# Kernel optimization log

Hardware: AMD Instinct MI355X
Metric: run time of the kernel (lower is better)

The kernel has to match this reference:

```python
import jax, jax.numpy as jnp
import numpy as np

PC = (-60.0, -60.0, -4.0, 140.0, 60.0, 4.0)
BEV_H, BEV_W, E, HEADS, LVLS, PTS, ZN, CAMS = 50, 50, 256, 8, 3, 4, 4, 6
HD = E // HEADS
IMG_H, IMG_W = 512.0, 800.0
SHAPES = ((64, 100), (32, 50), (16, 25))
FFN = 2 * E
EPS = 1e-5


def grid_sample(img, grid):
    # img (B,C,H,W), grid (B,Hg,Wg,2) in [-1,1]; bilinear, zeros padding, align_corners=False
    B, C, H, W = img.shape
    Hg, Wg = grid.shape[1], grid.shape[2]
    x = (grid[..., 0] + 1.0) * (W * 0.5) - 0.5
    y = (grid[..., 1] + 1.0) * (H * 0.5) - 0.5
    x0 = jnp.floor(x)
    y0 = jnp.floor(y)
    wx = x - x0
    wy = y - y0
    x0i = x0.astype(jnp.int32)
    y0i = y0.astype(jnp.int32)
    imgf = img.reshape(B, C, H * W)

    def gather(ix, iy):
        valid = ((ix >= 0) & (ix < W) & (iy >= 0) & (iy < H)).astype(img.dtype)
        idx = jnp.clip(iy, 0, H - 1) * W + jnp.clip(ix, 0, W - 1)
        idx = jnp.broadcast_to(idx.reshape(B, 1, Hg * Wg), (B, C, Hg * Wg))
        return jnp.take_along_axis(imgf, idx, axis=2).reshape(B, C, Hg, Wg) * valid[:, None]

    v00 = gather(x0i, y0i)
    v01 = gather(x0i + 1, y0i)
    v10 = gather(x0i, y0i + 1)
    v11 = gather(x0i + 1, y0i + 1)
    wx = wx[:, None]
    wy = wy[:, None]
    return v00 * (1 - wy) * (1 - wx) + v01 * (1 - wy) * wx + v10 * wy * (1 - wx) + v11 * wy * wx


def layer_norm(x, g, b):
    m = x.mean(-1, keepdims=True)
    v = ((x - m) ** 2).mean(-1, keepdims=True)
    return (x - m) / jnp.sqrt(v + 1e-5) * g + b


def get_reference_points():
    xs = (jnp.arange(BEV_W, dtype=jnp.float32) + 0.5) / BEV_W
    ys = (jnp.arange(BEV_H, dtype=jnp.float32) + 0.5) / BEV_H
    zs = (jnp.arange(ZN, dtype=jnp.float32) + 0.5) / ZN
    ref_y, ref_x = jnp.meshgrid(ys, xs, indexing='ij')
    xy = jnp.stack([ref_x, ref_y], -1).reshape(-1, 2)  # (HW,2)
    xy = jnp.broadcast_to(xy[:, None, :], (BEV_H * BEV_W, ZN, 2))
    z = jnp.broadcast_to(zs[None, :, None], (BEV_H * BEV_W, ZN, 1))
    r = jnp.concatenate([xy, z], -1)  # (HW,Z,3), normalized
    scale = jnp.array([PC[3] - PC[0], PC[4] - PC[1], PC[5] - PC[2]], jnp.float32)
    off = jnp.array([PC[0], PC[1], PC[2]], jnp.float32)
    return (r * scale + off).reshape(-1, 3)  # (HW*Z, 3)


def point_sampling(ref3d, l2i):
    # ref3d (Nq,3), l2i (B,N,4,4) -> ref2d (B,N,Nq,2), mask (B,N,Nq)
    Nq = ref3d.shape[0]
    pts = jnp.concatenate([ref3d, jnp.ones((Nq, 1), ref3d.dtype)], -1)
    cam = jnp.einsum('bnij,qj->bnqi', l2i, pts)
    d = cam[..., 2]
    u = cam[..., 0] / (d + EPS) / IMG_W
    v = cam[..., 1] / (d + EPS) / IMG_H
    ref2d = jnp.stack([u, v], -1)
    mask = (d > EPS) & (u > 0.0) & (u < 1.0) & (v > 0.0) & (v < 1.0)
    return ref2d, mask


def mha(q, k, v, fl):
    B = q.shape[0]
    wq, wk, wv = jnp.split(fl['ta_in_w'], 3, 0)
    bq, bk, bv = jnp.split(fl['ta_in_b'], 3, 0)
    Q = (q @ wq.T + bq).reshape(B, -1, HEADS, HD)
    K = (k @ wk.T + bk).reshape(B, -1, HEADS, HD)
    V = (v @ wv.T + bv).reshape(B, -1, HEADS, HD)
    a = jax.nn.softmax(jnp.einsum('bqhd,bkhd->bhqk', Q, K) / np.float32(np.sqrt(HD)), -1)
    o = jnp.einsum('bhqk,bkhd->bqhd', a, V).reshape(B, -1, E)
    return o @ fl['ta_out_w'].T + fl['ta_out_b']


def msda(query, qpos, value, ref, fl):
    # MultiScaleDeformableAttention (identity = zeros). ref (B,Nq,L,2) in [0,1].
    B, Nq, _ = query.shape
    q = query + qpos
    v = (value @ fl['vp_w'].T + fl['vp_b']).reshape(B, -1, HEADS, HD)
    off = (q @ fl['so_w'].T + fl['so_b']).reshape(B, Nq, HEADS, LVLS, PTS, 2)
    aw = jax.nn.softmax((q @ fl['aw_w'].T + fl['aw_b']).reshape(B, Nq, HEADS, LVLS * PTS), -1)
    aw = aw.reshape(B, Nq, HEADS, LVLS, PTS)
    norm = jnp.array([[w, h] for (h, w) in SHAPES], jnp.float32)  # (L,2) = (W,H)
    loc = ref[:, :, None, :, None, :] + off / norm[None, None, None, :, None, :]
    outs = []
    start = 0
    for l, (Hl, Wl) in enumerate(SHAPES):
        vl = v[:, start:start + Hl * Wl].transpose(0, 2, 3, 1).reshape(B * HEADS, HD, Hl, Wl)
        g = (2.0 * loc[:, :, :, l] - 1.0).transpose(0, 2, 1, 3, 4).reshape(B * HEADS, Nq, PTS, 2)
        outs.append(grid_sample(vl, g))  # (B*HEADS, HD, Nq, PTS)
        start += Hl * Wl
    s = jnp.stack(outs, 3)  # (B*HEADS, HD, Nq, L, P)
    w = aw.transpose(0, 2, 1, 3, 4).reshape(B * HEADS, 1, Nq, LVLS, PTS)
    o = (s * w).sum((3, 4)).reshape(B, HEADS, HD, Nq).transpose(0, 3, 1, 2).reshape(B, Nq, E)
    return o @ fl['op_w'].T + fl['op_b']


def spatial_attn(query, qpos, feats_t, l2i, ref3d, fl):
    B, Nq, _ = query.shape
    ref2d, mask = point_sampling(ref3d, l2i)
    out = jnp.zeros_like(query)
    valid = jnp.zeros((B, Nq), query.dtype)
    for cam in range(CAMS):
        value = jnp.concatenate(
            [f[:, cam].reshape(B, E, -1).transpose(0, 2, 1) for f in feats_t], axis=1)
        ref = jnp.broadcast_to(ref2d[:, cam][:, :, None, :], (B, Nq, LVLS, 2))
        a = msda(query, qpos, value, ref, fl)
        wgt = mask[:, cam].astype(query.dtype)
        out = out + a * wgt[..., None]
        valid = valid + wgt
    return out / jnp.maximum(valid, 1.0)[..., None]


def temporal_align(prev_bev, motion):
    B, C, H, W = prev_bev.shape
    xs = jnp.arange(W, dtype=prev_bev.dtype)
    ys = jnp.arange(H, dtype=prev_bev.dtype)
    yy, xx = jnp.meshgrid(ys, xs, indexing='ij')
    rx = (xx + 0.5) / W * (PC[3] - PC[0]) + PC[0]
    ry = (yy + 0.5) / H * (PC[4] - PC[1]) + PC[1]
    g = jnp.stack([rx, ry, jnp.zeros_like(rx), jnp.ones_like(rx)], -1)  # (H,W,4)
    inv = jnp.linalg.inv(motion)  # (B,4,4)
    gp = jnp.einsum('bij,hwj->bhwi', inv, g)
    nx = (gp[..., 0] - PC[0]) / (PC[3] - PC[0]) * 2.0 - 1.0
    ny = (gp[..., 1] - PC[1]) / (PC[4] - PC[1]) * 2.0 - 1.0
    return grid_sample(prev_bev, jnp.stack([nx, ny], -1))


def layer_fwd(bev, bev_pos, prev, feats_t, l2i, ref3d, fl):
    if prev is not None:
        attn = mha(bev + bev_pos, prev + bev_pos, prev, fl)
        bev = layer_norm(bev + attn, fl['n1_g'], fl['n1_b'])
    B, Nq, C = bev.shape
    bev_z = jnp.broadcast_to(bev[:, :, None, :], (B, Nq, ZN, C)).reshape(B, -1, C)
    pos_z = jnp.broadcast_to(bev_pos[:, :, None, :], (B, Nq, ZN, C)).reshape(B, -1, C)
    so = spatial_attn(bev_z, pos_z, feats_t, l2i, ref3d, fl)
    so = so.reshape(B, Nq, ZN, C).mean(2)
    bev = layer_norm(bev + so, fl['n2_g'], fl['n2_b'])
    h = jax.nn.relu(bev @ fl['ffn_w1'].T + fl['ffn_b1'])
    ffn = h @ fl['ffn_w2'].T + fl['ffn_b2']
    return layer_norm(bev + ffn, fl['n3_g'], fl['n3_b'])


def forward(fl, batch_size, seq_len):
    feats = [fl['feat0'], fl['feat1'], fl['feat2']]
    feats = [f.reshape(batch_size, seq_len, CAMS, E, f.shape[-2], f.shape[-1]) for f in feats]
    bev = jnp.broadcast_to(fl['bev_emb'][None], (batch_size, BEV_H * BEV_W, E))
    bev_pos = jnp.broadcast_to(fl['bev_pos_emb'][None], (batch_size, BEV_H * BEV_W, E))
    ref3d = get_reference_points()
    prev = None
    for t in range(seq_len):
        feats_t = [f[:, t] for f in feats]
        prev_al = None
        if prev is not None:
            pa = temporal_align(prev, fl['ego_motion'][:, t])
            prev_al = pa.reshape(batch_size, E, -1).transpose(0, 2, 1)
        bev_t = layer_fwd(bev, bev_pos, prev_al, feats_t, fl['lidar2img'][:, t], ref3d, fl)
        prev = bev_t.transpose(0, 2, 1).reshape(batch_size, E, BEV_H, BEV_W)
    return prev


def _make_cam_matrices():
    mats = np.zeros((CAMS, 4, 4), np.float32)
    K = np.array([[500.0, 0.0, 400.0], [0.0, 500.0, 256.0], [0.0, 0.0, 1.0]], np.float32)
    for i in range(CAMS):
        th = 2.0 * np.pi * i / CAMS
        xr = np.array([-np.sin(th), np.cos(th), 0.0])
        yr = np.array([0.0, 0.0, -1.0])
        fr = np.array([np.cos(th), np.sin(th), 0.0])
        R = np.stack([xr, yr, fr]).astype(np.float32)
        mats[i, :3, :3] = K @ R
        mats[i, 3, 3] = 1.0
    return mats


def setup_inputs() -> dict:
    key = jax.random.key(0)
    ks = jax.random.split(key, 20)
    rn = lambda k, s, sc=0.02: jax.random.normal(k, s, jnp.float32) * sc
    NOFF = HEADS * LVLS * PTS * 2
    NAW = HEADS * LVLS * PTS
    d = {
        'bev_emb': rn(ks[0], (BEV_H * BEV_W, E), 1.0),
        'bev_pos_emb': rn(ks[1], (BEV_H * BEV_W, E), 1.0),
        'ta_in_w': rn(ks[2], (3 * E, E)), 'ta_in_b': jnp.zeros(3 * E, jnp.float32),
        'ta_out_w': rn(ks[3], (E, E)), 'ta_out_b': jnp.zeros(E, jnp.float32),
        'so_w': rn(ks[4], (NOFF, E)), 'so_b': rn(ks[5], (NOFF,), 0.5),
        'aw_w': rn(ks[6], (NAW, E)), 'aw_b': jnp.zeros(NAW, jnp.float32),
        'vp_w': rn(ks[7], (E, E)), 'vp_b': jnp.zeros(E, jnp.float32),
        'op_w': rn(ks[8], (E, E)), 'op_b': jnp.zeros(E, jnp.float32),
        'ffn_w1': rn(ks[9], (FFN, E)), 'ffn_b1': jnp.zeros(FFN, jnp.float32),
        'ffn_w2': rn(ks[10], (E, FFN)), 'ffn_b2': jnp.zeros(E, jnp.float32),
        'n1_g': jnp.ones(E, jnp.float32), 'n1_b': jnp.zeros(E, jnp.float32),
        'n2_g': jnp.ones(E, jnp.float32), 'n2_b': jnp.zeros(E, jnp.float32),
        'n3_g': jnp.ones(E, jnp.float32), 'n3_b': jnp.zeros(E, jnp.float32),
        'feat0': rn(ks[11], (12, E, 64, 100), 1.0),
        'feat1': rn(ks[12], (12, E, 32, 50), 1.0),
        'feat2': rn(ks[13], (12, E, 16, 25), 1.0),
    }
    mats = _make_cam_matrices()  # realistic lidar->img projections per camera
    d['lidar2img'] = jnp.asarray(np.broadcast_to(mats, (1, 2, CAMS, 4, 4)).copy())
    em = np.tile(np.eye(4, dtype=np.float32), (1, 2, 1, 1))
    em[..., 0, 3] = 2.0  # 2m forward ego translation per step
    d['ego_motion'] = jnp.asarray(em)
    d['batch_size'] = 1
    d['seq_len'] = 2
    return d


def reference(bev_emb, bev_pos_emb, ta_in_w, ta_in_b, ta_out_w, ta_out_b,
              so_w, so_b, aw_w, aw_b, vp_w, vp_b, op_w, op_b,
              ffn_w1, ffn_b1, ffn_w2, ffn_b2,
              n1_g, n1_b, n2_g, n2_b, n3_g, n3_b,
              feat0, feat1, feat2, lidar2img, ego_motion, batch_size, seq_len):
    fl = dict(bev_emb=bev_emb, bev_pos_emb=bev_pos_emb, ta_in_w=ta_in_w, ta_in_b=ta_in_b,
              ta_out_w=ta_out_w, ta_out_b=ta_out_b, so_w=so_w, so_b=so_b, aw_w=aw_w, aw_b=aw_b,
              vp_w=vp_w, vp_b=vp_b, op_w=op_w, op_b=op_b, ffn_w1=ffn_w1, ffn_b1=ffn_b1,
              ffn_w2=ffn_w2, ffn_b2=ffn_b2, n1_g=n1_g, n1_b=n1_b, n2_g=n2_g, n2_b=n2_b,
              n3_g=n3_g, n3_b=n3_b, feat0=feat0, feat1=feat1, feat2=feat2,
              lidar2img=lidar2img, ego_motion=ego_motion)
    return forward(fl, int(batch_size), int(seq_len))
```

## Files before the change

### kernel.cpp

```cpp
#include <hip/hip_runtime.h>
#include <hip/hip_bf16.h>

#define NPIX   2500
#define EDIM   256
#define NHEADS 8
#define HDIM   32
#define NLVLS  3
#define NPTS   4
#define NZ     4
#define NCAMS  6
#define NQTOT  10000
#define NVAL   8400
#define FFND   512
#define NCHUNK 10
#define KVCH   250
#define VTROW  2504

typedef __attribute__((ext_vector_type(8))) short short8;
typedef __attribute__((ext_vector_type(4))) float float4v;

__device__ __forceinline__ void level_params(int l, int& H, int& W, int& st) {
    if (l == 0)      { H = 64; W = 100; st = 0;    }
    else if (l == 1) { H = 32; W = 50;  st = 6400; }
    else             { H = 16; W = 25;  st = 8000; }
// ... 88 lines not shown
        {
            const int gw = n0 + srow;
            if (gw < N) {
                const float* src = Wf + (size_t)gw * K + k0 + sk;
#pragma unroll
                for (int j = 0; j < 8; j++) tmp[j] = f2bf(src[j]);
            } else {
#pragma unroll
                for (int j = 0; j < 8; j++) tmp[j] = 0;
            }
            *(short8*)&Ws[srow][sk] = *(short8*)&tmp[0];
        }
        __syncthreads();
        short8 af[2], bfr[2];
#pragma unroll
        for (int mi = 0; mi < 2; mi++)
            af[mi] = *(const short8*)&As[wr * 32 + mi * 16 + fr][fk * 8];
#pragma unroll
        for (int ni = 0; ni < 2; ni++)
            bfr[ni] = *(const short8*)&Ws[wc * 32 + ni * 16 + fr][fk * 8];
#pragma unroll
        for (int mi = 0; mi < 2; mi++)
#pragma unroll
            for (int ni = 0; ni < 2; ni++)
                acc[mi][ni] = __builtin_amdgcn_mfma_f32_16x16x32_bf16(
                    af[mi], bfr[ni], acc[mi][ni], 0, 0, 0);
        __syncthreads();
    }
#pragma unroll
    for (int mi = 0; mi < 2; mi++)
#pragma unroll
        for (int ni = 0; ni < 2; ni++) {
            const int col = n0 + wc * 32 + ni * 16 + fr;
#pragma unroll
            for (int r = 0; r < 4; r++) {
                const int row = m0 + wr * 32 + mi * 16 + fk * 4 + r;
                if (row < M && col < N) {
                    float v = acc[mi][ni][r] + (Bf ? Bf[col] : 0.f);
                    if (ACT) v = fmaxf(v, 0.f);
                    Cb[(size_t)row * N + col] = v;
                }
            }
        }
}

template<int ACT, int ADD>
__global__ __launch_bounds__(256) void gemm64o_k(const float* __restrict__ A,
                                                 const float* __restrict__ A2,
                                                 const float* __restrict__ W,
                                                 const float* __restrict__ bias,
                                                 unsigned short* __restrict__ C,
                                                 int M, int N, int K)
{
    __shared__ unsigned short As[64][44];
    __shared__ unsigned short Ws[64][44];
    const int m0 = blockIdx.y * 64;
    const int n0 = blockIdx.x * 64;
    const int tid = threadIdx.x;
    const int wave = tid >> 6, lane = tid & 63;
    const int wr = wave >> 1, wc = wave & 1;
    const int fr = lane & 15, fk = lane >> 4;
    float4v acc[2][2];
#pragma unroll
    for (int mi = 0; mi < 2; mi++)
#pragma unroll
        for (int ni = 0; ni < 2; ni++) { acc[mi][ni][0] = 0.f; acc[mi][ni][1] = 0.f;
                                         acc[mi][ni][2] = 0.f; acc[mi][ni][3] = 0.f; }
    const int srow = tid >> 2, sk = (tid & 3) * 8;
    for (int k0 = 0; k0 < K; k0 += 32) {
        unsigned short tmp[8];
        {
            const int gr = m0 + srow;
            if (gr < M) {
                const float* src = A + (size_t)gr * K + k0 + sk;
                if (ADD) {
                    const float* src2 = A2 + (size_t)gr * K + k0 + sk;
#pragma unroll
                    for (int j = 0; j < 8; j++) tmp[j] = f2bf(src[j] + src2[j]);
                } else {
#pragma unroll
                    for (int j = 0; j < 8; j++) tmp[j] = f2bf(src[j]);
                }
            } else {
#pragma unroll
                for (int j = 0; j < 8; j++) tmp[j] = 0;
            }
            *(short8*)&As[srow][sk] = *(short8*)&tmp[0];
        }
        {
            const int gw = n0 + srow;
            if (gw < N) {
                const float* src = W + (size_t)gw * K + k0 + sk;
#pragma unroll
                for (int j = 0; j < 8; j++) tmp[j] = f2bf(src[j]);
            } else {
#pragma unroll
                for (int j = 0; j < 8; j++) tmp[j] = 0;
            }
            *(short8*)&Ws[srow][sk] = *(short8*)&tmp[0];
        }
        __syncthreads();
        short8 af[2], bfr[2];
#pragma unroll
        for (int mi = 0; mi < 2; mi++)
            af[mi] = *(const short8*)&As[wr * 32 + mi * 16 + fr][fk * 8];
#pragma unroll
        for (int ni = 0; ni < 2; ni++)
            bfr[ni] = *(const short8*)&Ws[wc * 32 + ni * 16 + fr][fk * 8];
#pragma unroll
        for (int mi = 0; mi < 2; mi++)
#pragma unroll
            for (int ni = 0; ni < 2; ni++)
                acc[mi][ni] = __builtin_amdgcn_mfma_f32_16x16x32_bf16(
                    af[mi], bfr[ni], acc[mi][ni], 0, 0, 0);
        __syncthreads();
    }
#pragma unroll
    for (int mi = 0; mi < 2; mi++)
#pragma unroll
        for (int ni = 0; ni < 2; ni++) {
            const int col = n0 + wc * 32 + ni * 16 + fr;
#pragma unroll
            for (int r = 0; r < 4; r++) {
                const int row = m0 + wr * 32 + mi * 16 + fk * 4 + r;
                if (row < M && col < N) {
                    float v = acc[mi][ni][r] + (bias ? bias[col] : 0.f);
                    if (ACT) v = fmaxf(v, 0.f);
                    C[(size_t)row * N + col] = f2bf(v);
                }
            }
        }
}

__global__ __launch_bounds__(256) void gemm_qkv_k(const float* __restrict__ bev_emb,
                                                  const float* __restrict__ prev_al,
                                                  const float* __restrict__ bev_pose,
                                                  const float* __restrict__ ta_in_w,
                                                  const float* __restrict__ ta_in_b,
                                                  unsigned short* __restrict__ Qbf,
                                                  unsigned short* __restrict__ Kbf,
                                                  unsigned short* __restrict__ VbfT)
{
    __shared__ unsigned short As[64][44];
    __shared__ unsigned short Ws[64][44];
    const int z = blockIdx.z;
    const float* A    = (z == 0) ? bev_emb : prev_al;
    const float* A2   = (z == 2) ? nullptr : bev_pose;
    const float* W    = ta_in_w + (size_t)z * EDIM * EDIM;
    const float* bias = ta_in_b + z * EDIM;
    const float oscale = (z == 0) ? 0.17677669529663689f : 1.0f;
    unsigned short* C = (z == 0) ? Qbf : (z == 1) ? Kbf : VbfT;
    const int m0 = blockIdx.y * 64;
    const int n0 = blockIdx.x * 64;
    const int tid = threadIdx.x;
    const int wave = tid >> 6, lane = tid & 63;
    const int wr = wave >> 1, wc = wave & 1;
    const int fr = lane & 15, fk = lane >> 4;
    float4v acc[2][2];
#pragma unroll
    for (int mi = 0; mi < 2; mi++)
#pragma unroll
        for (int ni = 0; ni < 2; ni++) { acc[mi][ni][0] = 0.f; acc[mi][ni][1] = 0.f;
                                         acc[mi][ni][2] = 0.f; acc[mi][ni][3] = 0.f; }
    const int srow = tid >> 2, sk = (tid & 3) * 8;
    for (int k0 = 0; k0 < EDIM; k0 += 32) {
        unsigned short tmp[8];
        {
            const int gr = m0 + srow;
            if (gr < NPIX) {
                const float* src = A + (size_t)gr * EDIM + k0 + sk;
                if (A2) {
                    const float* src2 = A2 + (size_t)gr * EDIM + k0 + sk;
#pragma unroll
                    for (int j = 0; j < 8; j++) tmp[j] = f2bf(src[j] + src2[j]);
                } else {
#pragma unroll
                    for (int j = 0; j < 8; j++) tmp[j] = f2bf(src[j]);
                }
            } else {
#pragma unroll
                for (int j = 0; j < 8; j++) tmp[j] = 0;
            }
            *(short8*)&As[srow][sk] = *(short8*)&tmp[0];
        }
        {
            const float* src = W + (size_t)(n0 + srow) * EDIM + k0 + sk;
#pragma unroll
            for (int j = 0; j < 8; j++) tmp[j] = f2bf(src[j]);
            *(short8*)&Ws[srow][sk] = *(short8*)&tmp[0];
        }
        __syncthreads();
        short8 af[2], bfr[2];
#pragma unroll
        for (int mi = 0; mi < 2; mi++)
            af[mi] = *(const short8*)&As[wr * 32 + mi * 16 + fr][fk * 8];
#pragma unroll
        for (int ni = 0; ni < 2; ni++)
            bfr[ni] = *(const short8*)&Ws[wc * 32 + ni * 16 + fr][fk * 8];
#pragma unroll
        for (int mi = 0; mi < 2; mi++)
#pragma unroll
            for (int ni = 0; ni < 2; ni++)
                acc[mi][ni] = __builtin_amdgcn_mfma_f32_16x16x32_bf16(
                    af[mi], bfr[ni], acc[mi][ni], 0, 0, 0);
        __syncthreads();
    }
#pragma unroll
    for (int mi = 0; mi < 2; mi++)
#pragma unroll
        for (int ni = 0; ni < 2; ni++) {
            const int col = n0 + wc * 32 + ni * 16 + fr;
#pragma unroll
            for (int r = 0; r < 4; r++) {
                const int row = m0 + wr * 32 + mi * 16 + fk * 4 + r;
                if (row < NPIX) {
                    const float v = (acc[mi][ni][r] + bias[col]) * oscale;
                    if (z == 2)
                        C[(size_t)col * VTROW + row] = f2bf(v);
                    else
                        C[(size_t)row * EDIM + col] = f2bf(v);
                }
            }
        }
}

__global__ __launch_bounds__(256) void gemm64b_k(const unsigned short* __restrict__ A,
                                                 const float* __restrict__ W,
                                                 const float* __restrict__ bias,
                                                 float* __restrict__ C,
                                                 int M, int N, int K,
                                                 size_t a_bs, size_t c_bs)
{
    __shared__ unsigned short As[64][44];
    __shared__ unsigned short Ws[64][44];
    const int m0 = blockIdx.y * 64;
    const int n0 = blockIdx.x * 64;
    const int tid = threadIdx.x;
    const unsigned short* Af = A + blockIdx.z * a_bs;
    float* Cb = C + blockIdx.z * c_bs;
    const int wave = tid >> 6, lane = tid & 63;
    const int wr = wave >> 1, wc = wave & 1;
    const int fr = lane & 15, fk = lane >> 4;
    float4v acc[2][2];
#pragma unroll
    for (int mi = 0; mi < 2; mi++)
#pragma unroll
        for (int ni = 0; ni < 2; ni++) { acc[mi][ni][0] = 0.f; acc[mi][ni][1] = 0.f;
                                         acc[mi][ni][2] = 0.f; acc[mi][ni][3] = 0.f; }
    const int srow = tid >> 2, sk = (tid & 3) * 8;
    for (int k0 = 0; k0 < K; k0 += 32) {
        {
            const int gr = m0 + srow;
            if (gr < M) {
                *(short8*)&As[srow][sk] =
                    *(const short8*)&Af[(size_t)gr * K + k0 + sk];
            } else {
                short8 z = {0,0,0,0,0,0,0,0};
                *(short8*)&As[srow][sk] = z;
            }
        }
        {
            unsigned short tmp[8];
            const int gw = n0 + srow;
            if (gw < N) {
                const float* src = W + (size_t)gw * K + k0 + sk;
#pragma unroll
                for (int j = 0; j < 8; j++) tmp[j] = f2bf(src[j]);
            } else {
#pragma unroll
                for (int j = 0; j < 8; j++) tmp[j] = 0;
            }
            *(short8*)&Ws[srow][sk] = *(short8*)&tmp[0];
        }
        __syncthreads();
        short8 af[2], bfr[2];
#pragma unroll
        for (int mi = 0; mi < 2; mi++)
            af[mi] = *(const short8*)&As[wr * 32 + mi * 16 + fr][fk * 8];
#pragma unroll
        for (int ni = 0; ni < 2; ni++)
            bfr[ni] = *(const short8*)&Ws[wc * 32 + ni * 16 + fr][fk * 8];
#pragma unroll
        for (int mi = 0; mi < 2; mi++)
#pragma unroll
            for (int ni = 0; ni < 2; ni++)
                acc[mi][ni] = __builtin_amdgcn_mfma_f32_16x16x32_bf16(
                    af[mi], bfr[ni], acc[mi][ni], 0, 0, 0);
        __syncthreads();
    }
#pragma unroll
    for (int mi = 0; mi < 2; mi++)
#pragma unroll
        for (int ni = 0; ni < 2; ni++) {
            const int col = n0 + wc * 32 + ni * 16 + fr;
#pragma unroll
            for (int r = 0; r < 4; r++) {
                const int row = m0 + wr * 32 + mi * 16 + fk * 4 + r;
                if (row < M && col < N)
                    Cb[(size_t)row * N + col] = acc[mi][ni][r] + (bias ? bias[col] : 0.f);
            }
        }
}

__global__ __launch_bounds__(256) void gemm_soaw_k(const float* __restrict__ A,
                                                   const float* __restrict__ A2,
                                                   const float* __restrict__ Wso,
                                                   const float* __restrict__ Waw,
                                                   const float* __restrict__ Bso,
                                                   const float* __restrict__ Baw,
                                                   float* __restrict__ C)
{
    __shared__ unsigned short As[64][44];
    __shared__ unsigned short Ws[64][44];
    const int m0 = blockIdx.y * 64;
    const int n0 = blockIdx.x * 64;
    const int tid = threadIdx.x;
    const int wave = tid >> 6, lane = tid & 63;
    const int wr = wave >> 1, wc = wave & 1;
    const int fr = lane & 15, fk = lane >> 4;
    float4v acc[2][2];
#pragma unroll
    for (int mi = 0; mi < 2; mi++)
#pragma unroll
        for (int ni = 0; ni < 2; ni++) { acc[mi][ni][0] = 0.f; acc[mi][ni][1] = 0.f;
                                         acc[mi][ni][2] = 0.f; acc[mi][ni][3] = 0.f; }
    const int srow = tid >> 2, sk = (tid & 3) * 8;
    for (int k0 = 0; k0 < EDIM; k0 += 32) {
        unsigned short tmp[8];
        {
            const int gr = m0 + srow;
            if (gr < NPIX) {
                const float* src  = A  + (size_t)gr * EDIM + k0 + sk;
                const float* src2 = A2 + (size_t)gr * EDIM + k0 + sk;
#pragma unroll
                for (int j = 0; j < 8; j++) tmp[j] = f2bf(src[j] + src2[j]);
            } else {
#pragma unroll
                for (int j = 0; j < 8; j++) tmp[j] = 0;
            }
            *(short8*)&As[srow][sk] = *(short8*)&tmp[0];
        }
        {
            const int gw = n0 + srow;
            const float* src = (gw < 192) ? Wso + (size_t)gw * EDIM + k0 + sk
                             : (gw < 288) ? Waw + (size_t)(gw - 192) * EDIM + k0 + sk
                                          : nullptr;
            if (src) {
#pragma unroll
                for (int j = 0; j < 8; j++) tmp[j] = f2bf(src[j]);
            } else {
#pragma unroll
                for (int j = 0; j < 8; j++) tmp[j] = 0;
            }
            *(short8*)&Ws[srow][sk] = *(short8*)&tmp[0];
        }
        __syncthreads();
        short8 af[2], bfr[2];
#pragma unroll
        for (int mi = 0; mi < 2; mi++)
            af[mi] = *(const short8*)&As[wr * 32 + mi * 16 + fr][fk * 8];
#pragma unroll
        for (int ni = 0; ni < 2; ni++)
            bfr[ni] = *(const short8*)&Ws[wc * 32 + ni * 16 + fr][fk * 8];
#pragma unroll
        for (int mi = 0; mi < 2; mi++)
#pragma unroll
            for (int ni = 0; ni < 2; ni++)
                acc[mi][ni] = __builtin_amdgcn_mfma_f32_16x16x32_bf16(
                    af[mi], bfr[ni], acc[mi][ni], 0, 0, 0);
        __syncthreads();
    }
#pragma unroll
    for (int mi = 0; mi < 2; mi++)
#pragma unroll
        for (int ni = 0; ni < 2; ni++) {
            const int col = n0 + wc * 32 + ni * 16 + fr;
#pragma unroll
            for (int r = 0; r < 4; r++) {
                const int row = m0 + wr * 32 + mi * 16 + fk * 4 + r;
                if (row < NPIX && col < 288) {
                    const float b = (col < 192) ? Bso[col] : Baw[col - 192];
                    C[(size_t)row * 288 + col] = acc[mi][ni][r] + b;
                }
            }
        }
}

template<int TRANS>
__global__ __launch_bounds__(256) void resid_ln_k(const float* __restrict__ x0,
                                                  const float* __restrict__ x1,
                                                  const float* __restrict__ cvec,
                                                  const float* __restrict__ cscale,
                                                  const float* __restrict__ g,
                                                  const float* __restrict__ bta,
                                                  float* __restrict__ out)
{
    const int row = blockIdx.x, e = threadIdx.x;
    float x = x0[(size_t)row * EDIM + e] + x1[(size_t)row * EDIM + e];
    if (cvec) x += cvec[e] * cscale[row];
    __shared__ float red[256];
    red[e] = x; __syncthreads();
    for (int s = 128; s > 0; s >>= 1) { if (e < s) red[e] += red[e + s]; __syncthreads(); }
    float mean = red[0] * (1.f / 256.f);
    __syncthreads();
    float dx = x - mean;
    red[e] = dx * dx; __syncthreads();
    for (int s = 128; s > 0; s >>= 1) { if (e < s) red[e] += red[e + s]; __syncthreads(); }
    float var = red[0] * (1.f / 256.f);
    const float res = dx * rsqrtf(var + 1e-5f) * g[e] + bta[e];
    if (TRANS)
        out[(size_t)e * NPIX + row] = res;
    else
        out[(size_t)row * EDIM + e] = res;
}

__global__ void uv_aw_k(const float* __restrict__ l2i, int t,
                        const float* __restrict__ raw,
                        float* __restrict__ uvtab,
                        float* __restrict__ validn,
                        float* __restrict__ aw_soft)
{
    if (blockIdx.x < 40) {
        const int n = blockIdx.x * 256 + threadIdx.x;
        if (n >= NQTOT) return;
        const int pix = n >> 2, iz = n & 3;
        const int prow = pix / 50, pcol = pix % 50;
        const float x3 = (pcol + 0.5f) * 4.0f - 60.f;
        const float y3 = (prow + 0.5f) * 2.4f - 60.f;
        const float z3 = (iz + 0.5f) * 2.0f - 4.f;
        int vcount = 0;
        float buf[12];
#pragma unroll
        for (int cam = 0; cam < NCAMS; cam++) {
            const float* Mt = l2i + (size_t)(t * NCAMS + cam) * 16;
            const float p0 = Mt[0] * x3 + Mt[1] * y3 + Mt[2]  * z3 + Mt[3];
            const float p1 = Mt[4] * x3 + Mt[5] * y3 + Mt[6]  * z3 + Mt[7];
            const float p2 = Mt[8] * x3 + Mt[9] * y3 + Mt[10] * z3 + Mt[11];
            const float dd = p2 + 1e-5f;
            const float u = p0 / dd * (1.f / 800.f);
            const float v = p1 / dd * (1.f / 512.f);
            const bool valid = (p2 > 1e-5f) && (u > 0.f) && (u < 1.f) &&
                               (v > 0.f) && (v < 1.f);
            if (valid) vcount++;
            buf[cam * 2]     = valid ? u : -1.f;
            buf[cam * 2 + 1] = v;
        }
#pragma unroll
        for (int j = 0; j < 12; j++) uvtab[(size_t)n * 12 + j] = buf[j];
        validn[n] = (float)vcount;
    } else {
        const int gidx = (blockIdx.x - 40) * 256 + threadIdx.x;
        if (gidx >= NPIX * NHEADS) return;
        const int pix = gidx / NHEADS, h = gidx % NHEADS;
        const float* p = raw + (size_t)pix * 288 + 192 + h * 12;
        float m = -3.0e38f;
#pragma unroll
        for (int j = 0; j < 12; j++) m = fmaxf(m, p[j]);
        float e[12]; float s = 0.f;
#pragma unroll
        for (int j = 0; j < 12; j++) { e[j] = __expf(p[j] - m); s += e[j]; }
        const float inv = 1.f / s;
        float* o = aw_soft + (size_t)pix * 96 + h * 12;
#pragma unroll
        for (int j = 0; j < 12; j++) o[j] = e[j] * inv;
    }
}

__global__ __launch_bounds__(256) void spatial_sample_k(const float* __restrict__ vproj,
                                                        const float* __restrict__ offb,
                                                        const float* __restrict__ awb,
                                                        const float* __restrict__ uvtab,
                                                        float* __restrict__ S)
{
    const int n = blockIdx.x;
    const int tid = threadIdx.x;
    const int wave = tid >> 6, lane = tid & 63;
    const int ch0 = lane << 2;
    const int h = lane >> 3;
    const int pix = n >> 2;
    __shared__ float soff[192];
    __shared__ float saw[96];
    __shared__ float suv[12];
    __shared__ float red[3][256];
    if (tid < 192) soff[tid] = offb[(size_t)pix * 288 + tid];
    if (tid < 96)  saw[tid]  = awb[(size_t)pix * 96 + tid];
    if (tid >= 192 && tid < 204) suv[tid - 192] = uvtab[(size_t)n * 12 + (tid - 192)];
    __syncthreads();
    float4 acc = make_float4(0.f, 0.f, 0.f, 0.f);
    for (int cam = 0; cam < NCAMS; cam++) {
        const float u = suv[cam * 2];
        if (u < 0.f) continue;
        const float v = suv[cam * 2 + 1];
        const float* vc = vproj + (size_t)cam * NVAL * EDIM + ch0;
        for (int pt = wave; pt < NLVLS * NPTS; pt += 4) {
            const int l = pt >> 2, p = pt & 3;
            int Hl, Wl, st; level_params(l, Hl, Wl, st);
            const int ob = ((h * NLVLS + l) * NPTS + p) * 2;
            const float x = u * (float)Wl + soff[ob]     - 0.5f;
            const float y = v * (float)Hl + soff[ob + 1] - 0.5f;
            const float xf = floorf(x), yf = floorf(y);
            const float wx = x - xf, wy = y - yf;
            const int x0 = (int)xf, y0 = (int)yf;
            const float a = saw[(h * NLVLS + l) * NPTS + p];
            const bool xi0 = (x0 >= 0) & (x0 < Wl);
            const bool xi1 = (x0 + 1 >= 0) & (x0 + 1 < Wl);
            const bool yi0 = (y0 >= 0) & (y0 < Hl);
            const bool yi1 = (y0 + 1 >= 0) & (y0 + 1 < Hl);
            const int rb = st + y0 * Wl + x0;
            float4 sv = make_float4(0.f, 0.f, 0.f, 0.f);
            if (yi0 & xi0) {
                const float w00 = (1.f - wy) * (1.f - wx);
                const float4 t4 = *(const float4*)(vc + ((size_t)rb << 8));
                sv.x += w00 * t4.x; sv.y += w00 * t4.y; sv.z += w00 * t4.z; sv.w += w00 * t4.w;
            }
            if (yi0 & xi1) {
                const float w01 = (1.f - wy) * wx;
                const float4 t4 = *(const float4*)(vc + ((size_t)(rb + 1) << 8));
                sv.x += w01 * t4.x; sv.y += w01 * t4.y; sv.z += w01 * t4.z; sv.w += w01 * t4.w;
            }
            if (yi1 & xi0) {
                const float w10 = wy * (1.f - wx);
                const float4 t4 = *(const float4*)(vc + ((size_t)(rb + Wl) << 8));
                sv.x += w10 * t4.x; sv.y += w10 * t4.y; sv.z += w10 * t4.z; sv.w += w10 * t4.w;
            }
            if (yi1 & xi1) {
                const float w11 = wy * wx;
                const float4 t4 = *(const float4*)(vc + ((size_t)(rb + Wl + 1) << 8));
                sv.x += w11 * t4.x; sv.y += w11 * t4.y; sv.z += w11 * t4.z; sv.w += w11 * t4.w;
            }
            acc.x += a * sv.x; acc.y += a * sv.y; acc.z += a * sv.z; acc.w += a * sv.w;
        }
    }
    if (wave > 0) *(float4*)&red[wave - 1][ch0] = acc;
    __syncthreads();
    if (wave == 0) {
#pragma unroll
        for (int w2 = 0; w2 < 3; w2++) {
            const float4 r4 = *(const float4*)&red[w2][ch0];
            acc.x += r4.x; acc.y += r4.y; acc.z += r4.z; acc.w += r4.w;
        }
        *(float4*)(S + (size_t)n * EDIM + ch0) = acc;
    }
}

__global__ __launch_bounds__(256) void reduce_z_k(const float* __restrict__ S,
                                                  const float* __restrict__ validn,
                                                  unsigned short* __restrict__ Smbf,
                                                  float* __restrict__ vbm)
{
    const int pix = blockIdx.x, e = threadIdx.x;
    float s = 0.f, vb = 0.f;
#pragma unroll
    for (int iz = 0; iz < NZ; iz++) {
        int n = pix * NZ + iz;
        float vn = validn[n];
        float inv = 1.f / fmaxf(vn, 1.f);
        s += S[(size_t)n * EDIM + e] * inv;
        vb += (vn > 0.f) ? 1.f : 0.f;
    }
    Smbf[(size_t)pix * EDIM + e] = f2bf(s * 0.25f);
    if (e == 0) vbm[pix] = vb * 0.25f;
}

__global__ __launch_bounds__(256) void talign_k(const float* __restrict__ prev,
                                                const float* __restrict__ motion,
                                                float* __restrict__ out)
{
    __shared__ float sinv[16];
    if (threadIdx.x == 0) {
        float a[4][8];
        for (int i = 0; i < 4; i++)
            for (int j = 0; j < 4; j++) { a[i][j] = motion[i * 4 + j];
                                          a[i][4 + j] = (i == j) ? 1.f : 0.f; }
        for (int col = 0; col < 4; col++) {
            int piv = col;
            for (int r = col + 1; r < 4; r++)
                if (fabsf(a[r][col]) > fabsf(a[piv][col])) piv = r;
            if (piv != col)
                for (int j = 0; j < 8; j++) { float tp = a[col][j];
                                              a[col][j] = a[piv][j]; a[piv][j] = tp; }
            float idv = 1.f / a[col][col];
            for (int j = 0; j < 8; j++) a[col][j] *= idv;
            for (int r = 0; r < 4; r++) {
                if (r == col) continue;
                float f = a[r][col];
                for (int j = 0; j < 8; j++) a[r][j] -= f * a[col][j];
            }
        }
        for (int i = 0; i < 4; i++)
            for (int j = 0; j < 4; j++) sinv[i * 4 + j] = a[i][4 + j];
    }
    __syncthreads();
    const int pix = blockIdx.x, e = threadIdx.x;
    const int r = pix / 50, c = pix % 50;
    const float rx = (c + 0.5f) * 4.0f - 60.f;
    const float ry = (r + 0.5f) * 2.4f - 60.f;
    const float gx = sinv[0] * rx + sinv[1] * ry + sinv[3];
    const float gy = sinv[4] * rx + sinv[5] * ry + sinv[7];
    const float nx = (gx + 60.f) * 0.01f - 1.f;
    const float ny = (gy + 60.f) * (1.f / 60.f) - 1.f;
    const float x = (nx + 1.f) * 25.f - 0.5f;
    const float y = (ny + 1.f) * 25.f - 0.5f;
    const float xf = floorf(x), yf = floorf(y);
    const float wx = x - xf, wy = y - yf;
    const int x0 = (int)xf, y0 = (int)yf;
    bool xi0 = (x0 >= 0 && x0 < 50), xi1 = (x0 + 1 >= 0 && x0 + 1 < 50);
    bool yi0 = (y0 >= 0 && y0 < 50), yi1 = (y0 + 1 >= 0 && y0 + 1 < 50);
    float s = 0.f;
    if (yi0 && xi0) s += (1.f - wy) * (1.f - wx) * prev[(size_t)(y0 * 50 + x0) * EDIM + e];
    if (yi0 && xi1) s += (1.f - wy) * wx         * prev[(size_t)(y0 * 50 + x0 + 1) * EDIM + e];
    if (yi1 && xi0) s += wy * (1.f - wx)         * prev[(size_t)((y0 + 1) * 50 + x0) * EDIM + e];
    if (yi1 && xi1) s += wy * wx                 * prev[(size_t)((y0 + 1) * 50 + x0 + 1) * EDIM + e];
    out[(size_t)pix * EDIM + e] = s;
}

__global__ __launch_bounds__(256) void mha_mfma_k(const unsigned short* __restrict__ Qbf,
                                                  const unsigned short* __restrict__ Kbf,
                                                  const unsigned short* __restrict__ VbfT,
                                                  float* __restrict__ pacc,
                                                  float* __restrict__ pml)
{
    const int h = blockIdx.y;
    const int q0 = blockIdx.x * 64;
    const int chunk = blockIdx.z;
    const int kv0 = chunk * KVCH;
    const int kv1 = min(NPIX, kv0 + KVCH);
    const int tid = threadIdx.x;
    const int wave = tid >> 6, lane = tid & 63;
    const int fr = lane & 15, fk = lane >> 4;

    __shared__ unsigned short Qs[64][44];
    __shared__ unsigned short Ks[64][44];
    __shared__ unsigned short Vt[32][76];
    __shared__ unsigned short Ps[4][16][76];

    const int srow = tid >> 2, scs = tid & 3;
    {
        const int gq = q0 + srow;
        if (gq < NPIX)
            *(short8*)&Qs[srow][scs * 8] =
                *(const short8*)&Qbf[(size_t)gq * EDIM + h * HDIM + scs * 8];
        else {
            short8 z = {0,0,0,0,0,0,0,0};
            *(short8*)&Qs[srow][scs * 8] = z;
        }
    }
    __syncthreads();
    const short8 aq = *(const short8*)&Qs[wave * 16 + fr][fk * 8];

    float m[4], l[4];
    float4v o0, o1;
#pragma unroll
    for (int r = 0; r < 4; r++) { m[r] = -3.0e38f; l[r] = 0.f; o0[r] = 0.f; o1[r] = 0.f; }

    const int vd = tid >> 3, vpart = tid & 7;
    for (int kb = kv0; kb < kv1; kb += 64) {
        __syncthreads();
        {
            const int gk = kb + srow;
            if (gk < kv1)
                *(short8*)&Ks[srow][scs * 8] =
                    *(const short8*)&Kbf[(size_t)gk * EDIM + h * HDIM + scs * 8];
            else {
                short8 z = {0,0,0,0,0,0,0,0};
                *(short8*)&Ks[srow][scs * 8] = z;
            }
            const unsigned short* vrow = VbfT + (size_t)(h * HDIM + vd) * VTROW;
            const int base = kb + vpart * 8;
            if (base + 8 <= kv1) {
                *(short8*)&Vt[vd][vpart * 8] = *(const short8*)&vrow[base];
            } else {
#pragma unroll
                for (int j = 0; j < 8; j++)
                    Vt[vd][vpart * 8 + j] = (base + j < kv1) ? vrow[base + j] : 0;
            }
        }
        __syncthreads();
        float4v s[4];
#pragma unroll
        for (int t = 0; t < 4; t++) {
            const short8 bk = *(const short8*)&Ks[t * 16 + fr][fk * 8];
            float4v z; z[0] = 0.f; z[1] = 0.f; z[2] = 0.f; z[3] = 0.f;
            s[t] = __builtin_amdgcn_mfma_f32_16x16x32_bf16(aq, bk, z, 0, 0, 0);
        }
        if (kb + 64 > kv1) {
#pragma unroll
            for (int t = 0; t < 4; t++) {
                const int colg = kb + t * 16 + fr;
                if (colg >= kv1) { s[t][0] = -3.0e38f; s[t][1] = -3.0e38f;
                                   s[t][2] = -3.0e38f; s[t][3] = -3.0e38f; }
            }
        }
        float cand[4];
#pragma unroll
        for (int r = 0; r < 4; r++)
            cand[r] = fmaxf(fmaxf(s[0][r], s[1][r]), fmaxf(s[2][r], s[3][r]));
#pragma unroll
        for (int off = 1; off < 16; off <<= 1)
#pragma unroll
            for (int r = 0; r < 4; r++)
                cand[r] = fmaxf(cand[r], __shfl_xor(cand[r], off));
        float corr[4];
#pragma unroll
        for (int r = 0; r < 4; r++) {
            const float mn = fmaxf(m[r], cand[r]);
            corr[r] = __expf(m[r] - mn);
            m[r] = mn;
        }
        float psum[4];
#pragma unroll
        for (int r = 0; r < 4; r++) psum[r] = 0.f;
#pragma unroll
        for (int t = 0; t < 4; t++)
#pragma unroll
            for (int r = 0; r < 4; r++) {
                const float p = __expf(s[t][r] - m[r]);
                psum[r] += p;
                Ps[wave][fk * 4 + r][t * 16 + fr] = f2bf(p);
            }
#pragma unroll
        for (int off = 1; off < 16; off <<= 1)
#pragma unroll
            for (int r = 0; r < 4; r++)
                psum[r] += __shfl_xor(psum[r], off);
#pragma unroll
        for (int r = 0; r < 4; r++) {
            l[r] = l[r] * corr[r] + psum[r];
            o0[r] *= corr[r];
            o1[r] *= corr[r];
        }
        const short8 ap0 = *(const short8*)&Ps[wave][fr][fk * 8];
        const short8 ap1 = *(const short8*)&Ps[wave][fr][32 + fk * 8];
        {
            const short8 bv0 = *(const short8*)&Vt[fr][fk * 8];
            const short8 bv1 = *(const short8*)&Vt[fr][32 + fk * 8];
            o0 = __builtin_amdgcn_mfma_f32_16x16x32_bf16(ap0, bv0, o0, 0, 0, 0);
            o0 = __builtin_amdgcn_mfma_f32_16x16x32_bf16(ap1, bv1, o0, 0, 0, 0);
        }
        {
            const short8 bv0 = *(const short8*)&Vt[16 + fr][fk * 8];
            const short8 bv1 = *(const short8*)&Vt[16 + fr][32 + fk * 8];
            o1 = __builtin_amdgcn_mfma_f32_16x16x32_bf16(ap0, bv0, o1, 0, 0, 0);
            o1 = __builtin_amdgcn_mfma_f32_16x16x32_bf16(ap1, bv1, o1, 0, 0, 0);
        }
    }
#pragma unroll
    for (int r = 0; r < 4; r++) {
        const int q = q0 + wave * 16 + fk * 4 + r;
        if (q < NPIX) {
            const size_t pi = ((size_t)chunk * NPIX + q) * NHEADS + h;
            pacc[pi * 32 + fr]      = o0[r];
            pacc[pi * 32 + 16 + fr] = o1[r];
            if (fr == 0) { pml[pi * 2] = m[r]; pml[pi * 2 + 1] = l[r]; }
        }
    }
}

__global__ __launch_bounds__(256) void mha_merge_k(const float* __restrict__ pacc,
                                                   const float* __restrict__ pml,
                                                   unsigned short* __restrict__ O)
{
    const int q = blockIdx.x;
    const int tid = threadIdx.x;
    const int h = tid >> 5, d = tid & 31;
    float ms[NCHUNK], ls[NCHUNK];
    float gm = -3.0e38f;
#pragma unroll
    for (int c = 0; c < NCHUNK; c++) {
        const size_t pi = ((size_t)c * NPIX + q) * NHEADS + h;
        ms[c] = pml[pi * 2];
        ls[c] = pml[pi * 2 + 1];
        gm = fmaxf(gm, ms[c]);
    }
    float gl = 0.f, s = 0.f;
#pragma unroll
    for (int c = 0; c < NCHUNK; c++) {
        const size_t pi = ((size_t)c * NPIX + q) * NHEADS + h;
        float w = __expf(ms[c] - gm);
        gl += ls[c] * w;
        s  += pacc[pi * 32 + d] * w;
    }
    O[(size_t)q * EDIM + h * HDIM + d] = f2bf(s / gl);
}

extern "C" void kernel_launch(void* const* d_in, const int* in_sizes, int n_in,
                              void* d_out, int out_size, void* d_ws, size_t ws_size,
                              hipStream_t stream)
{
    const float* bev_emb  = (const float*)d_in[0];
    const float* bev_pose = (const float*)d_in[1];
    const float* ta_in_w  = (const float*)d_in[2];
    const float* ta_in_b  = (const float*)d_in[3];
    const float* ta_out_w = (const float*)d_in[4];
    const float* ta_out_b = (const float*)d_in[5];
    const float* so_w     = (const float*)d_in[6];
    const float* so_b     = (const float*)d_in[7];
    const float* aw_w     = (const float*)d_in[8];
    const float* aw_b     = (const float*)d_in[9];
    const float* vp_w     = (const float*)d_in[10];
    const float* vp_b     = (const float*)d_in[11];
    const float* op_w     = (const float*)d_in[12];
    const float* op_b     = (const float*)d_in[13];
    const float* ffn_w1   = (const float*)d_in[14];
    const float* ffn_b1   = (const float*)d_in[15];
    const float* ffn_w2   = (const float*)d_in[16];
    const float* ffn_b2   = (const float*)d_in[17];
    const float* n1_g     = (const float*)d_in[18];
    const float* n1_b     = (const float*)d_in[19];
    const float* n2_g     = (const float*)d_in[20];
    const float* n2_b     = (const float*)d_in[21];
    const float* n3_g     = (const float*)d_in[22];
    const float* n3_b     = (const float*)d_in[23];
    const float* feat0    = (const float*)d_in[24];
    const float* feat1    = (const float*)d_in[25];
    const float* feat2    = (const float*)d_in[26];
    const float* l2i      = (const float*)d_in[27];
    const float* ego      = (const float*)d_in[28];

    float* w = (float*)d_ws;
    float* ws_inv   = w;
    float* validn   = w + 16;
    float* vbm      = w + 10016;
    float* bev_cur  = w + 16384;
    float* bev_prev = bev_cur  + 640000;
    float* qin      = bev_prev + 640000;
    float* kin      = qin      + 640000;
    float* prev_al  = kin      + 640000;
    float* Qb       = prev_al  + 640000;
    float* Kb       = Qb       + 640000;
    float* Vb       = Kb       + 640000;
    float* attn_pre = Vb       + 640000;
    float* attn_o   = attn_pre + 640000;
    float* off_buf  = attn_o   + 640000;
    float* aw_raw   = off_buf  + 480000;
    float* aw_soft  = aw_raw   + 240000;
    float* Sm       = aw_soft  + 240000;
    float* vproj    = Sm       + 640000;
    float* Sbuf     = Qb;
    float* ffn_h    = kin;
    float* pacc     = vproj;
    float* pml      = vproj + (size_t)NCHUNK * NPIX * NHEADS * 32;
    unsigned short* featT = (unsigned short*)qin;
    float* uvtab = attn_o;
    unsigned short* Qbf  = (unsigned short*)attn_o;
    unsigned short* Kbf  = Qbf + 640000;
    unsigned short* VbfT = (unsigned short*)off_buf;
    unsigned short* Smbf = (unsigned short*)Sm;
    unsigned short* attn_pre_bf = (unsigned short*)attn_pre;
    unsigned short* ffn_hbf = (unsigned short*)ffn_h;
    (void)aw_raw; (void)Qb; (void)Kb; (void)Vb; (void)ws_inv;

    auto GEMM = [&](const float* A, const float* Wp, const float* bias, float* C,
                    int M, int N, int K, int act) {
        dim3 g((N + 63) / 64, (M + 63) / 64);
        if (act)
            gemm64_k<1, 0><<<g, 256, 0, stream>>>(A, nullptr, Wp, bias, C, M, N, K,
                                                  0, 0, 0, 0);
        else
            gemm64_k<0, 0><<<g, 256, 0, stream>>>(A, nullptr, Wp, bias, C, M, N, K,
                                                  0, 0, 0, 0);
    };

    for (int t = 0; t < 2; t++) {
        const float* cur = bev_emb;
        if (t > 0) {
            talign_k<<<NPIX, 256, 0, stream>>>(bev_prev, ego + (size_t)t * 16, prev_al);
            gemm_qkv_k<<<dim3(4, 40, 3), 256, 0, stream>>>(
                bev_emb, prev_al, bev_pose, ta_in_w, ta_in_b, Qbf, Kbf, VbfT);
            mha_mfma_k<<<dim3((NPIX + 63) / 64, NHEADS, NCHUNK), 256, 0, stream>>>(
                Qbf, Kbf, VbfT, pacc, pml);
            mha_merge_k<<<NPIX, 256, 0, stream>>>(pacc, pml, attn_pre_bf);
            gemm64b_k<<<dim3(4, 40), 256, 0, stream>>>(
                attn_pre_bf, ta_out_w, ta_out_b, attn_o, NPIX, EDIM, EDIM, 0, 0);
            resid_ln_k<0><<<NPIX, 256, 0, stream>>>(bev_emb, attn_o, nullptr, nullptr,
                                                    n1_g, n1_b, bev_cur);
            cur = bev_cur;
        }
        transpose_feat_all_k<<<dim3(263, 8, 6), 256, 0, stream>>>(
            feat0, feat1, feat2, t, featT);
        gemm64b_k<<<dim3(4, 132, 6), 256, 0, stream>>>(
            featT, vp_w, vp_b, vproj, NVAL, EDIM, EDIM,
            (size_t)NVAL * EDIM, (size_t)NVAL * EDIM);
        gemm_soaw_k<<<dim3(5, 40), 256, 0, stream>>>(cur, bev_pose, so_w, aw_w,
                                                     so_b, aw_b, off_buf);
        uv_aw_k<<<119, 256, 0, stream>>>(l2i, t, off_buf, uvtab, validn, aw_soft);
        spatial_sample_k<<<NQTOT, 256, 0, stream>>>(vproj, off_buf, aw_soft, uvtab, Sbuf);
        reduce_z_k<<<NPIX, 256, 0, stream>>>(Sbuf, validn, Smbf, vbm);
        gemm64b_k<<<dim3(4, 40), 256, 0, stream>>>(
            Smbf, op_w, nullptr, attn_o, NPIX, EDIM, EDIM, 0, 0);
        resid_ln_k<0><<<NPIX, 256, 0, stream>>>(cur, attn_o, op_b, vbm,
                                                n2_g, n2_b, bev_cur);
        gemm64o_k<1, 0><<<dim3(8, 40), 256, 0, stream>>>(
            bev_cur, nullptr, ffn_w1, ffn_b1, ffn_hbf, NPIX, FFND, EDIM);
        gemm64b_k<<<dim3(4, 40), 256, 0, stream>>>(
            ffn_hbf, ffn_w2, ffn_b2, attn_o, NPIX, EDIM, FFND, 0, 0);
        if (t == 0)
            resid_ln_k<0><<<NPIX, 256, 0, stream>>>(bev_cur, attn_o, nullptr, nullptr,
                                                    n3_g, n3_b, bev_prev);
        else
            resid_ln_k<1><<<NPIX, 256, 0, stream>>>(bev_cur, attn_o, nullptr, nullptr,
                                                    n3_g, n3_b, (float*)d_out);
    }
}
```

Before: 408.7 us.

## Fuse value-proj with offset GEMM and fold z-reduction into output-proj GEMM

The value-projection GEMM over six cameras and the sampling-offset/attention-weight GEMM now share one launch, using grid z-slices to select the problem and early-returning the unused blocks. The z-reduction kernel is removed: the output-projection GEMM now loads the four z-samples per pixel, scales each by its inverse valid count and averages them while staging the A tile. The valid-BEV mask is computed in uv_aw_k with lane shuffles. This saves launches and an intermediate bf16 buffer round trip, but the output GEMM reads four times as much fp32 A data per tile, and many blocks of the fused grid exit immediately.

Measured after the change: 390.2 us (median of 2 runs). 1.05x faster.

```diff
diff --git a/kernel.cpp b/kernel.cpp
--- a/kernel.cpp
+++ b/kernel.cpp
@@ -414,14 +414,22 @@
         }
 }
 
-__global__ __launch_bounds__(256) void gemm_soaw_k(const float* __restrict__ A,
-                                                   const float* __restrict__ A2,
-                                                   const float* __restrict__ Wso,
-                                                   const float* __restrict__ Waw,
-                                                   const float* __restrict__ Bso,
-                                                   const float* __restrict__ Baw,
-                                                   float* __restrict__ C)
-{
+__global__ __launch_bounds__(256) void gemm_vs_k(const unsigned short* __restrict__ featT,
+                                                 const float* __restrict__ vp_w,
+                                                 const float* __restrict__ vp_b,
+                                                 float* __restrict__ vproj,
+                                                 const float* __restrict__ Aso,
+                                                 const float* __restrict__ A2so,
+                                                 const float* __restrict__ Wso,
+                                                 const float* __restrict__ Waw,
+                                                 const float* __restrict__ Bso,
+                                                 const float* __restrict__ Baw,
+                                                 float* __restrict__ Cso)
+{
+    const int z = blockIdx.z;
+    const bool so = (z == 6);
+    if (!so && blockIdx.x >= 4) return;
+    if (so && blockIdx.y >= 40) return;
     __shared__ unsigned short As[64][44];
     __shared__ unsigned short Ws[64][44];
     const int m0 = blockIdx.y * 64;
@@ -430,6 +438,8 @@
     const int wave = tid >> 6, lane = tid & 63;
     const int wr = wave >> 1, wc = wave & 1;
     const int fr = lane & 15, fk = lane >> 4;
+    const unsigned short* Af = featT + (size_t)z * NVAL * EDIM;
+    const int M = so ? NPIX : NVAL;
     float4v acc[2][2];
 #pragma unroll
     for (int mi = 0; mi < 2; mi++)
@@ -441,22 +451,36 @@
         unsigned short tmp[8];
         {
             const int gr = m0 + srow;
-            if (gr < NPIX) {
-                const float* src  = A  + (size_t)gr * EDIM + k0 + sk;
-                const float* src2 = A2 + (size_t)gr * EDIM + k0 + sk;
-#pragma unroll
-                for (int j = 0; j < 8; j++) tmp[j] = f2bf(src[j] + src2[j]);
+            if (so) {
+                if (gr < NPIX) {
+                    const float* src  = Aso  + (size_t)gr * EDIM + k0 + sk;
+                    const float* src2 = A2so + (size_t)gr * EDIM + k0 + sk;
+#pragma unroll
+                    for (int j = 0; j < 8; j++) tmp[j] = f2bf(src[j] + src2[j]);
+                } else {
+#pragma unroll
+                    for (int j = 0; j < 8; j++) tmp[j] = 0;
+                }
+                *(short8*)&As[srow][sk] = *(short8*)&tmp[0];
             } else {
-#pragma unroll
-                for (int j = 0; j < 8; j++) tmp[j] = 0;
-            }
-            *(short8*)&As[srow][sk] = *(short8*)&tmp[0];
+                if (gr < NVAL) {
+                    *(short8*)&As[srow][sk] =
+                        *(const short8*)&Af[(size_t)gr * EDIM + k0 + sk];
+                } else {
+                    short8 zr = {0,0,0,0,0,0,0,0};
+                    *(short8*)&As[srow][sk] = zr;
+                }
+            }
         }
         {
             const int gw = n0 + srow;
-            const float* src = (gw < 192) ? Wso + (size_t)gw * EDIM + k0 + sk
-                             : (gw < 288) ? Waw + (size_t)(gw - 192) * EDIM + k0 + sk
-                                          : nullptr;
+            const float* src;
+            if (so)
+                src = (gw < 192) ? Wso + (size_t)gw * EDIM + k0 + sk
+                    : (gw < 288) ? Waw + (size_t)(gw - 192) * EDIM + k0 + sk
+                                 : nullptr;
+            else
+                src = vp_w + (size_t)gw * EDIM + k0 + sk;
             if (src) {
 #pragma unroll
                 for (int j = 0; j < 8; j++) tmp[j] = f2bf(src[j]);
@@ -490,10 +514,103 @@
 #pragma unroll
             for (int r = 0; r < 4; r++) {
                 const int row = m0 + wr * 32 + mi * 16 + fk * 4 + r;
-                if (row < NPIX && col < 288) {
-                    const float b = (col < 192) ? Bso[col] : Baw[col - 192];
-                    C[(size_t)row * 288 + col] = acc[mi][ni][r] + b;
+                if (row < M) {
+                    if (so) {
+                        if (col < 288) {
+                            const float b = (col < 192) ? Bso[col] : Baw[col - 192];
+                            Cso[(size_t)row * 288 + col] = acc[mi][ni][r] + b;
+                        }
+                    } else {
+                        vproj[((size_t)z * NVAL + row) * EDIM + col] =
+                            acc[mi][ni][r] + vp_b[col];
+                    }
                 }
+            }
+        }
+}
+
+__global__ __launch_bounds__(256) void gemm_op_k(const float* __restrict__ S,
+                                                 const float* __restrict__ validn,
+                                                 const float* __restrict__ W,
+                                                 float* __restrict__ C)
+{
+    __shared__ unsigned short As[64][44];
+    __shared__ unsigned short Ws[64][44];
+    __shared__ float sfac[256];
+    const int m0 = blockIdx.y * 64;
+    const int n0 = blockIdx.x * 64;
+    const int tid = threadIdx.x;
+    {
+        const int idx = m0 * 4 + tid;
+        const float vn = (idx < NQTOT) ? validn[idx] : 1.f;
+        sfac[tid] = 1.f / fmaxf(vn, 1.f);
+    }
+    __syncthreads();
+    const int wave = tid >> 6, lane = tid & 63;
+    const int wr = wave >> 1, wc = wave & 1;
+    const int fr = lane & 15, fk = lane >> 4;
+    float4v acc[2][2];
+#pragma unroll
+    for (int mi = 0; mi < 2; mi++)
+#pragma unroll
+        for (int ni = 0; ni < 2; ni++) { acc[mi][ni][0] = 0.f; acc[mi][ni][1] = 0.f;
+                                         acc[mi][ni][2] = 0.f; acc[mi][ni][3] = 0.f; }
+    const int srow = tid >> 2, sk = (tid & 3) * 8;
+    for (int k0 = 0; k0 < EDIM; k0 += 32) {
+        unsigned short tmp[8];
+        {
+            const int gr = m0 + srow;
+            if (gr < NPIX) {
+                float sum[8];
+#pragma unroll
+                for (int j = 0; j < 8; j++) sum[j] = 0.f;
+#pragma unroll
+                for (int iz = 0; iz < NZ; iz++) {
+                    const float* src = S + ((size_t)(gr * 4 + iz) * EDIM + k0 + sk);
+                    const float f = sfac[srow * 4 + iz];
+#pragma unroll
+                    for (int j = 0; j < 8; j++) sum[j] += src[j] * f;
+                }
+#pragma unroll
+                for (int j = 0; j < 8; j++) tmp[j] = f2bf(sum[j] * 0.25f);
+            } else {
+#pragma unroll
+                for (int j = 0; j < 8; j++) tmp[j] = 0;
+            }
+            *(short8*)&As[srow][sk] = *(short8*)&tmp[0];
+        }
+        {
+            const float* src = W + (size_t)(n0 + srow) * EDIM + k0 + sk;
+#pragma unroll
+            for (int j = 0; j < 8; j++) tmp[j] = f2bf(src[j]);
+            *(short8*)&Ws[srow][sk] = *(short8*)&tmp[0];
+        }
+        __syncthreads();
+        short8 af[2], bfr[2];
+#pragma unroll
+        for (int mi = 0; mi < 2; mi++)
+            af[mi] = *(const short8*)&As[wr * 32 + mi * 16 + fr][fk * 8];
+#pragma unroll
+        for (int ni = 0; ni < 2; ni++)
+            bfr[ni] = *(const short8*)&Ws[wc * 32 + ni * 16 + fr][fk * 8];
+#pragma unroll
+        for (int mi = 0; mi < 2; mi++)
+#pragma unroll
+            for (int ni = 0; ni < 2; ni++)
+                acc[mi][ni] = __builtin_amdgcn_mfma_f32_16x16x32_bf16(
+                    af[mi], bfr[ni], acc[mi][ni], 0, 0, 0);
+        __syncthreads();
+    }
+#pragma unroll
+    for (int mi = 0; mi < 2; mi++)
+#pragma unroll
+        for (int ni = 0; ni < 2; ni++) {
+            const int col = n0 + wc * 32 + ni * 16 + fr;
+#pragma unroll
+            for (int r = 0; r < 4; r++) {
+                const int row = m0 + wr * 32 + mi * 16 + fk * 4 + r;
+                if (row < NPIX)
+                    C[(size_t)row * EDIM + col] = acc[mi][ni][r];
             }
         }
 }
@@ -530,7 +647,8 @@
                         const float* __restrict__ raw,
                         float* __restrict__ uvtab,
                         float* __restrict__ validn,
-                        float* __restrict__ aw_soft)
+                        float* __restrict__ aw_soft,
+                        float* __restrict__ vbm)
 {
     if (blockIdx.x < 40) {
         const int n = blockIdx.x * 256 + threadIdx.x;
@@ -560,6 +678,10 @@
 #pragma unroll
         for (int j = 0; j < 12; j++) uvtab[(size_t)n * 12 + j] = buf[j];
         validn[n] = (float)vcount;
+        float ind = (vcount > 0) ? 1.f : 0.f;
+        ind += __shfl_xor(ind, 1);
+        ind += __shfl_xor(ind, 2);
+        if (iz == 0) vbm[pix] = ind * 0.25f;
     } else {
         const int gidx = (blockIdx.x - 40) * 256 + threadIdx.x;
         if (gidx >= NPIX * NHEADS) return;
@@ -655,25 +777,6 @@
     }
 }
 
-__global__ __launch_bounds__(256) void reduce_z_k(const float* __restrict__ S,
-                                                  const float* __restrict__ validn,
-                                                  unsigned short* __restrict__ Smbf,
-                                                  float* __restrict__ vbm)
-{
-    const int pix = blockIdx.x, e = threadIdx.x;
-    float s = 0.f, vb = 0.f;
-#pragma unroll
-    for (int iz = 0; iz < NZ; iz++) {
-        int n = pix * NZ + iz;
-        float vn = validn[n];
-        float inv = 1.f / fmaxf(vn, 1.f);
-        s += S[(size_t)n * EDIM + e] * inv;
-        vb += (vn > 0.f) ? 1.f : 0.f;
-    }
-    Smbf[(size_t)pix * EDIM + e] = f2bf(s * 0.25f);
-    if (e == 0) vbm[pix] = vb * 0.25f;
-}
-
 __global__ __launch_bounds__(256) void talign_k(const float* __restrict__ prev,
                                                 const float* __restrict__ motion,
                                                 float* __restrict__ out)
@@ -957,10 +1060,9 @@
     unsigned short* Qbf  = (unsigned short*)attn_o;
     unsigned short* Kbf  = Qbf + 640000;
     unsigned short* VbfT = (unsigned short*)off_buf;
-    unsigned short* Smbf = (unsigned short*)Sm;
     unsigned short* attn_pre_bf = (unsigned short*)attn_pre;
     unsigned short* ffn_hbf = (unsigned short*)ffn_h;
-    (void)aw_raw; (void)Qb; (void)Kb; (void)Vb; (void)ws_inv;
+    (void)aw_raw; (void)Qb; (void)Kb; (void)Vb; (void)ws_inv; (void)Sm;
 
     auto GEMM = [&](const float* A, const float* Wp, const float* bias, float* C,
                     int M, int N, int K, int act) {
@@ -990,16 +1092,11 @@
         }
         transpose_feat_all_k<<<dim3(263, 8, 6), 256, 0, stream>>>(
             feat0, feat1, feat2, t, featT);
-        gemm64b_k<<<dim3(4, 132, 6), 256, 0, stream>>>(
-            featT, vp_w, vp_b, vproj, NVAL, EDIM, EDIM,
-            (size_t)NVAL * EDIM, (size_t)NVAL * EDIM);
-        gemm_soaw_k<<<dim3(5, 40), 256, 0, stream>>>(cur, bev_pose, so_w, aw_w,
-                                                     so_b, aw_b, off_buf);
-        uv_aw_k<<<119, 256, 0, stream>>>(l2i, t, off_buf, uvtab, validn, aw_soft);
+        gemm_vs_k<<<dim3(5, 132, 7), 256, 0, stream>>>(
+            featT, vp_w, vp_b, vproj, cur, bev_pose, so_w, aw_w, so_b, aw_b, off_buf);
+        uv_aw_k<<<119, 256, 0, stream>>>(l2i, t, off_buf, uvtab, validn, aw_soft, vbm);
         spatial_sample_k<<<NQTOT, 256, 0, stream>>>(vproj, off_buf, aw_soft, uvtab, Sbuf);
-        reduce_z_k<<<NPIX, 256, 0, stream>>>(Sbuf, validn, Smbf, vbm);
-        gemm64b_k<<<dim3(4, 40), 256, 0, stream>>>(
-            Smbf, op_w, nullptr, attn_o, NPIX, EDIM, EDIM, 0, 0);
+        gemm_op_k<<<dim3(4, 40), 256, 0, stream>>>(Sbuf, validn, op_w, attn_o);
         resid_ln_k<0><<<NPIX, 256, 0, stream>>>(cur, attn_o, op_b, vbm,
                                                 n2_g, n2_b, bev_cur);
         gemm64o_k<1, 0><<<dim3(8, 40), 256, 0, stream>>>(
```
